# Performance work log

Hardware: AMD Instinct MI355X
Metric: run time of the kernel (lower is better)

Reference implementation:

```python
import jax, jax.numpy as jnp
import numpy as np

N_NODES = 50000
N_EDGES = 800000
IN_FEATS = 256
N_HEADS = 4
OUT_FEATS = 32
NEG_SLOPE = 0.2


def setup_inputs() -> dict:
    key = jax.random.key(0)
    k_feat, k_src, k_dst, k_fc, k_al, k_ar, k_res = jax.random.split(key, 7)
    feat = jax.random.normal(k_feat, (N_NODES, IN_FEATS), dtype=jnp.float32)
    src = jax.random.randint(k_src, (N_EDGES,), 0, N_NODES)
    dst = jax.random.randint(k_dst, (N_EDGES,), 0, N_NODES)
    # xavier-normal-ish scales
    s_fc = (2.0 / (IN_FEATS + N_HEADS * OUT_FEATS)) ** 0.5
    W_fc = jax.random.normal(k_fc, (N_HEADS * OUT_FEATS, IN_FEATS), dtype=jnp.float32) * s_fc
    s_a = (2.0 / (1 + N_HEADS * OUT_FEATS)) ** 0.5
    attn_l = jax.random.normal(k_al, (N_HEADS, OUT_FEATS), dtype=jnp.float32) * s_a
    attn_r = jax.random.normal(k_ar, (N_HEADS, OUT_FEATS), dtype=jnp.float32) * s_a
    W_res = jax.random.normal(k_res, (N_HEADS * OUT_FEATS, IN_FEATS), dtype=jnp.float32) * s_fc
    return {"feat": feat, "src": src, "dst": dst, "W_fc": W_fc,
            "attn_l": attn_l, "attn_r": attn_r, "W_res": W_res}


def reference(feat, src, dst, W_fc, attn_l, attn_r, W_res):
    N = feat.shape[0]
    H, D = attn_l.shape
    ones_e = jnp.ones(src.shape[0], dtype=feat.dtype)

    # projection: [N, H, D]
    h = (feat @ W_fc.T).reshape(N, H, D)
    feat_dst = h  # dst features are pre-norm (torch code aliases before * norm)

    # symmetric norm on source side: out_degree^-0.5
    out_deg = jax.ops.segment_sum(ones_e, src, num_segments=N)
    feat_src = h * (jnp.clip(out_deg, 1.0) ** -0.5)[:, None, None]

    # per-node attention halves -> per-edge score, leaky relu
    el = jnp.einsum('nhd,hd->nh', feat_src, attn_l)  # [N, H]
    er = jnp.einsum('nhd,hd->nh', feat_dst, attn_r)  # [N, H]
    e = jax.nn.leaky_relu(el[src] + er[dst], NEG_SLOPE)  # [E, H]

    # edge_softmax over incoming edges of each dst node
    emax = jax.ops.segment_max(e, dst, num_segments=N)
    emax = jnp.where(jnp.isfinite(emax), emax, 0.0)  # guard empty segments
    ex = jnp.exp(e - emax[dst])
    denom = jax.ops.segment_sum(ex, dst, num_segments=N)
    a = ex / denom[dst]  # [E, H]

    # weighted scatter-sum of messages: u_mul_e + sum
    msg = feat_src[src] * a[:, :, None]  # [E, H, D]
    rst = jax.ops.segment_sum(msg, dst, num_segments=N)  # [N, H, D]

    # symmetric norm on destination side: in_degree^0.5
    in_deg = jax.ops.segment_sum(ones_e, dst, num_segments=N)
    rst = rst * jnp.sqrt(jnp.clip(in_deg, 1.0))[:, None, None]

    # residual projection
    rst = rst + (feat @ W_res.T).reshape(N, H, D)
    return rst
```

## Files before the change

### kernel.cpp

```cpp
#include <hip/hip_runtime.h>
#include <hip/hip_bf16.h>
#include <math.h>

#define HD 128
#define IN_F 256
#define NEG_SLOPE 0.2f
#define NMAX 50000
#define GGRID 256
#define CSRC 32

typedef __attribute__((ext_vector_type(8))) short short8;
typedef __attribute__((ext_vector_type(4))) float f32x4;

__device__ __forceinline__ unsigned short f2bf(float x) {
    __hip_bfloat16 b = __float2bfloat16(x);
    return *(unsigned short*)&b;
}
__device__ __forceinline__ float bf2f(unsigned short u) {
    unsigned int v = ((unsigned int)u) << 16;
    float f;
    __builtin_memcpy(&f, &v, 4);
    return f;
}
__device__ __forceinline__ short8 pack8(float4 f0, float4 f1) {
    short8 v;
    v[0] = (short)f2bf(f0.x); v[1] = (short)f2bf(f0.y);
    v[2] = (short)f2bf(f0.z); v[3] = (short)f2bf(f0.w);
    v[4] = (short)f2bf(f1.x); v[5] = (short)f2bf(f1.y);
    v[6] = (short)f2bf(f1.z); v[7] = (short)f2bf(f1.w);
    return v;
}

__global__ __launch_bounds__(1024) void hist_cvt_kernel(
    const int* __restrict__ src, const int* __restrict__ dst,
    unsigned short* __restrict__ pc_src, unsigned short* __restrict__ pc_dst,
    const float4* __restrict__ wfc4, const float4* __restrict__ wres4,
    const float* __restrict__ wfc, const float* __restrict__ attn_l,
    const float* __restrict__ attn_r, ushort4* __restrict__ w16,
    unsigned short* __restrict__ ew16, int n4each,
    int N, int E, int C, int chunk, int chunk_s) {
    __shared__ unsigned int h[NMAX / 2];
    int tid = threadIdx.x;
    int b = blockIdx.x;

    if (b >= C + CSRC) {
        int rb = b - C - CSRC;
        if (rb == 0) {
            int hh = tid >> 8, k = tid & 255;
            float sl = 0.f, sr = 0.f;
#pragma unroll 8
            for (int d = 0; d < 32; d++) {
                float w = wfc[(size_t)(hh * 32 + d) * IN_F + k];
                sl += attn_l[hh * 32 + d] * w;
                sr += attn_r[hh * 32 + d] * w;
            }
            ew16[hh * IN_F + k] = f2bf(sl);
            ew16[(4 + hh) * IN_F + k] = f2bf(sr);
            ew16[(8 + hh) * IN_F + k] = 0;
            ew16[(12 + hh) * IN_F + k] = 0;
        } else {
            int idx = (rb - 1) * 1024 + tid;
            if (idx < 2 * n4each) {
                float4 f = (idx < n4each) ? wfc4[idx] : wres4[idx - n4each];
                ushort4 u;
                u.x = f2bf(f.x); u.y = f2bf(f.y); u.z = f2bf(f.z); u.w = f2bf(f.w);
                w16[idx] = u;
            }
        }
        return;
    }

    int nh = N >> 1;
    uint4* h4 = (uint4*)h;
    for (int i = tid; i < (nh >> 2); i += 1024) h4[i] = make_uint4(0, 0, 0, 0);
    for (int i = (nh & ~3) + tid; i < nh; i += 1024) h[i] = 0;
    __syncthreads();

    bool isSrc = (b >= C);
    const int* arr = isSrc ? src : dst;
    int c = isSrc ? (b - C) : b;
    int ch = isSrc ? chunk_s : chunk;
    int e0 = c * ch, e1 = min(E, (c + 1) * ch);
    for (int e = e0 + tid; e < e1; e += 1024) {
        int v = arr[e];
        atomicAdd(&h[v >> 1], 1u << ((v & 1) << 4));
    }
    __syncthreads();

    unsigned short* pc = (isSrc ? pc_src : pc_dst) + (size_t)c * N;
    uint4* pc4 = (uint4*)pc;
    for (int i = tid; i < (nh >> 2); i += 1024) pc4[i] = h4[i];
    for (int i = (nh & ~3) + tid; i < nh; i += 1024) ((unsigned int*)pc)[i] = h[i];
}

__global__ __launch_bounds__(256) void sum_scan1_kernel(
    const unsigned short* __restrict__ pc_src, unsigned short* __restrict__ pc_dst,
    int* __restrict__ out_cnt, int* __restrict__ deg, int* __restrict__ bsum,
    int N, int C) {
    __shared__ int wsum[4];
    int n = blockIdx.x * 256 + threadIdx.x;
    int sd = 0;
    if (n < N) {
        int ss = 0;
#pragma unroll 4
        for (int c = 0; c < CSRC; c++) ss += pc_src[(size_t)c * N + n];
        for (int c = 0; c < C; c++) {
            unsigned short v = pc_dst[(size_t)c * N + n];
            pc_dst[(size_t)c * N + n] = (unsigned short)sd;
            sd += v;
        }
        out_cnt[n] = ss;
        deg[n] = sd;
    }
    int v = (n < N) ? sd : 0;
#pragma unroll
    for (int d = 1; d < 64; d <<= 1) v += __shfl_xor(v, d);
    if ((threadIdx.x & 63) == 0) wsum[threadIdx.x >> 6] = v;
    __syncthreads();
    if (threadIdx.x == 0) bsum[blockIdx.x] = wsum[0] + wsum[1] + wsum[2] + wsum[3];
}

__global__ __launch_bounds__(256) void scan3_kernel(const int* __restrict__ deg,
                                                    const int* __restrict__ bsum,
                                                    int* __restrict__ row_start,
                                                    int N, int nb, int E) {
    __shared__ int wsum[4];
    __shared__ int sbo[256];
    int tid = threadIdx.x, lane = tid & 63, wid = tid >> 6;
    {
        int v = (tid < nb) ? bsum[tid] : 0;
        int incl = v;
#pragma unroll
        for (int d = 1; d < 64; d <<= 1) {
            int t = __shfl_up(incl, d);
            if (lane >= d) incl += t;
        }
        if (lane == 63) wsum[wid] = incl;
        __syncthreads();
        int woff = 0;
        for (int w = 0; w < wid; w++) woff += wsum[w];
        sbo[tid] = woff + incl - v;
        __syncthreads();
    }
    int boff = sbo[blockIdx.x];
    if (blockIdx.x == 0 && tid == 0) row_start[N] = E;
    __syncthreads();

    int i = blockIdx.x * 256 + tid;
    int v = (i < N) ? deg[i] : 0;
    int incl = v;
#pragma unroll
    for (int d = 1; d < 64; d <<= 1) {
        int t = __shfl_up(incl, d);
        if (lane >= d) incl += t;
    }
    if (lane == 63) wsum[wid] = incl;
    __syncthreads();
    int woff = 0;
    for (int w = 0; w < wid; w++) woff += wsum[w];
    int excl = boff + woff + incl - v;
    if (i < N) row_start[i] = excl;
}

__global__ __launch_bounds__(1024, 1) void place_gemm_kernel(
    const int* __restrict__ src, const int* __restrict__ dst,
    const unsigned short* __restrict__ chunkpre, const int* __restrict__ row_start,
    int* __restrict__ esrc,
    const float* __restrict__ feat, const __hip_bfloat16* __restrict__ w16,
    const __hip_bfloat16* __restrict__ ew16, const int* __restrict__ out_cnt,
    unsigned short* __restrict__ h16, unsigned short* __restrict__ resid16,
    float* __restrict__ el, float* __restrict__ er,
    int N, int E, int C, int chunk, int ntiles) {
    __shared__ __align__(16) char smem[147456];
    int tid = threadIdx.x;

    if (blockIdx.x < C) {
        unsigned int* cur = (unsigned int*)smem;
        int nh = N >> 1;
        const unsigned short* cp = chunkpre + (size_t)blockIdx.x * N;
        const uint4* cp4 = (const uint4*)cp;
        uint4* cur4 = (uint4*)cur;
        for (int i = tid; i < (nh >> 2); i += 1024) cur4[i] = cp4[i];
        for (int i = (nh & ~3) + tid; i < nh; i += 1024)
            cur[i] = ((const unsigned int*)cp)[i];
        __syncthreads();

        int e1 = min(E, (int)(blockIdx.x + 1) * chunk);
        for (int e = blockIdx.x * chunk + tid; e < e1; e += 1024) {
            int d = dst[e], s = src[e];
            int sh = (d & 1) << 4;
            unsigned int old = atomicAdd(&cur[d >> 1], 1u << sh);
            int rank = (old >> sh) & 0xffff;
            esrc[row_start[d] + rank] = s;
        }
        return;
    }

    unsigned short* sB = (unsigned short*)smem;
    unsigned short* sA = (unsigned short*)(smem + 131072);
    int bid = blockIdx.x - C;
    int lane = tid & 63, w = tid >> 6;
    int l15 = lane & 15, lg = lane >> 4;
    int c0 = w * 16;
    bool w0 = (w == 0);
    bool isH = (w < 8);
    int colloc = c0 & 127;

#pragma unroll
    for (int it = 0; it < 8; ++it) {
        int idx = it * 1024 + tid;
        int c = idx >> 5, g = idx & 31;
        short8 v = *(const short8*)(w16 + (size_t)c * IN_F + g * 8);
        *(short8*)&sB[c * 256 + ((g ^ (c & 7)) * 8)] = v;
    }
    short8 ereg[8];
    if (w0) {
        const __hip_bfloat16* ep = ew16 + (size_t)l15 * IN_F + lg * 8;
#pragma unroll
        for (int kk = 0; kk < 8; kk++) ereg[kk] = *(const short8*)(ep + kk * 32);
    }

    int srow = tid >> 5, sgc = tid & 31;
    float4 fA0, fA1;
    int t = bid;
    {
        int gm = t * 32 + srow;
        gm = (gm < N) ? gm : (N - 1);
        const float4* fp = (const float4*)(feat + (size_t)gm * IN_F + sgc * 8);
        fA0 = fp[0];
        fA1 = fp[1];
    }

    for (; t < ntiles; t += GGRID) {
        __syncthreads();
        *(short8*)&sA[srow * 256 + ((sgc ^ (srow & 7)) * 8)] = pack8(fA0, fA1);
        __syncthreads();

        int tn = t + GGRID;
        if (tn < ntiles) {
            int gm = tn * 32 + srow;
            gm = (gm < N) ? gm : (N - 1);
            const float4* fp = (const float4*)(feat + (size_t)gm * IN_F + sgc * 8);
            fA0 = fp[0];
            fA1 = fp[1];
        }

        f32x4 acc[2], accE[2];
#pragma unroll
        for (int i = 0; i < 2; i++) {
            acc[i] = (f32x4){0.f, 0.f, 0.f, 0.f};
            accE[i] = (f32x4){0.f, 0.f, 0.f, 0.f};
        }
#pragma unroll
        for (int kk = 0; kk < 8; kk++) {
            short8 a[2], b;
#pragma unroll
            for (int mi = 0; mi < 2; mi++) {
                int row = mi * 16 + l15;
                int gs = (kk * 4 + lg) ^ (row & 7);
                a[mi] = *(const short8*)&sA[row * 256 + gs * 8];
            }
            {
                int c = c0 + l15;
                int gsb = (kk * 4 + lg) ^ (c & 7);
                b = *(const short8*)&sB[c * 256 + gsb * 8];
            }
#pragma unroll
            for (int mi = 0; mi < 2; mi++)
                acc[mi] = __builtin_amdgcn_mfma_f32_16x16x32_bf16(a[mi], b, acc[mi],
                                                                  0, 0, 0);
            if (w0) {
#pragma unroll
                for (int mi = 0; mi < 2; mi++)
                    accE[mi] = __builtin_amdgcn_mfma_f32_16x16x32_bf16(
                        a[mi], ereg[kk], accE[mi], 0, 0, 0);
            }
        }

        int bm = t * 32;
#pragma unroll
        for (int mi = 0; mi < 2; mi++) {
#pragma unroll
            for (int reg = 0; reg < 4; reg++) {
                int r = bm + mi * 16 + lg * 4 + reg;
                bool valid = (r < N);
                int rr = valid ? r : 0;
                if (isH) {
                    float nrm = rsqrtf(fmaxf((float)out_cnt[rr], 1.0f));
                    if (valid) {
                        h16[(size_t)r * HD + colloc + l15] = f2bf(acc[mi][reg] * nrm);
                        if (w0) {
                            float ev = accE[mi][reg];
                            if (l15 < 4) el[r * 4 + l15] = ev * nrm;
                            else if (l15 < 8) er[r * 4 + (l15 - 4)] = ev;
                        }
                    }
                } else if (valid) {
                    resid16[(size_t)r * HD + colloc + l15] = f2bf(acc[mi][reg]);
                }
            }
        }
    }
}

__global__ __launch_bounds__(256) void agg_kernel(const unsigned short* __restrict__ h16,
                                                  const float* __restrict__ el,
                                                  const float* __restrict__ er,
                                                  const int* __restrict__ row_start,
                                                  const int* __restrict__ esrc,
                                                  const unsigned short* __restrict__ resid16,
                                                  float* __restrict__ out, int N) {
    int wid = threadIdx.x >> 6, lane = threadIdx.x & 63;
    int n = blockIdx.x * 4 + wid;
    if (n >= N) return;
    int es = lane >> 4;
    int l15 = lane & 15;
    int h = l15 >> 2;
    int d0 = l15 * 8;
    int beg = row_start[n], end = row_start[n + 1];
    float erh = er[n * 4 + h];
    float den = 0.f;
    float acc[8];
#pragma unroll
    for (int j = 0; j < 8; j++) acc[j] = 0.f;

    if (beg < end) {
        bool ok0, ok1;
        float ev0, ev1; short8 hv0, hv1;
        {
            int i0 = beg + es, i1 = beg + 4 + es;
            ok0 = i0 < end; ok1 = i1 < end;
            int s0 = esrc[ok0 ? i0 : beg];
            int s1 = esrc[ok1 ? i1 : beg];
            ev0 = el[s0 * 4 + h]; ev1 = el[s1 * 4 + h];
            hv0 = *(const short8*)(h16 + (size_t)s0 * HD + d0);
            hv1 = *(const short8*)(h16 + (size_t)s1 * HD + d0);
        }
        for (int base = beg + 8; base < end; base += 8) {
            int i0 = base + es, i1 = base + 4 + es;
            bool p0 = i0 < end, p1 = i1 < end;
            int t0 = esrc[p0 ? i0 : beg];
            int t1 = esrc[p1 ? i1 : beg];
            float fv0 = el[t0 * 4 + h];
            float fv1 = el[t1 * 4 + h];
            short8 g0 = *(const short8*)(h16 + (size_t)t0 * HD + d0);
            short8 g1 = *(const short8*)(h16 + (size_t)t1 * HD + d0);
            float e0 = ev0 + erh; e0 = (e0 > 0.f) ? e0 : NEG_SLOPE * e0;
            float e1 = ev1 + erh; e1 = (e1 > 0.f) ? e1 : NEG_SLOPE * e1;
            float ex0 = ok0 ? __expf(e0) : 0.f;
            float ex1 = ok1 ? __expf(e1) : 0.f;
            den += ex0 + ex1;
#pragma unroll
            for (int j = 0; j < 8; j++)
                acc[j] += ex0 * bf2f((unsigned short)hv0[j]) +
                          ex1 * bf2f((unsigned short)hv1[j]);
            ok0 = p0; ok1 = p1; ev0 = fv0; ev1 = fv1; hv0 = g0; hv1 = g1;
        }
        float e0 = ev0 + erh; e0 = (e0 > 0.f) ? e0 : NEG_SLOPE * e0;
        float e1 = ev1 + erh; e1 = (e1 > 0.f) ? e1 : NEG_SLOPE * e1;
        float ex0 = ok0 ? __expf(e0) : 0.f;
        float ex1 = ok1 ? __expf(e1) : 0.f;
        den += ex0 + ex1;
#pragma unroll
        for (int j = 0; j < 8; j++)
            acc[j] += ex0 * bf2f((unsigned short)hv0[j]) +
                      ex1 * bf2f((unsigned short)hv1[j]);
    }

#pragma unroll
    for (int m = 16; m < 64; m <<= 1) {
        den += __shfl_xor(den, m);
#pragma unroll
        for (int j = 0; j < 8; j++) acc[j] += __shfl_xor(acc[j], m);
    }

    if (es == 0) {
        const unsigned short* rp = resid16 + (size_t)n * HD + d0;
        short8 rv = *(const short8*)rp;
        int indeg = end - beg;
        float sc = (indeg > 0) ? sqrtf((float)indeg) / den : 0.f;
        float o[8];
#pragma unroll
        for (int j = 0; j < 8; j++)
            o[j] = sc * acc[j] + bf2f((unsigned short)rv[j]);
        float* op = out + (size_t)n * HD + d0;
        *(float4*)op = make_float4(o[0], o[1], o[2], o[3]);
        *(float4*)(op + 4) = make_float4(o[4], o[5], o[6], o[7]);
    }
}

extern "C" void kernel_launch(void* const* d_in, const int* in_sizes, int n_in,
                              void* d_out, int out_size, void* d_ws, size_t ws_size,
                              hipStream_t stream) {
    const float* feat   = (const float*)d_in[0];
    const int*   src    = (const int*)d_in[1];
    const int*   dst    = (const int*)d_in[2];
    const float* W_fc   = (const float*)d_in[3];
    const float* attn_l = (const float*)d_in[4];
    const float* attn_r = (const float*)d_in[5];
    const float* W_res  = (const float*)d_in[6];
    float* out = (float*)d_out;

    int N = in_sizes[0] / IN_F;
    int E = in_sizes[1];
    int nb = (N + 255) / 256;

    size_t off = 0;
    auto alloc = [&](size_t bytes) {
        size_t o = off;
        off = (off + bytes + 255) & ~(size_t)255;
        return o;
    };
    char* ws = (char*)d_ws;
    unsigned short* h16     = (unsigned short*)(ws + alloc((size_t)N * HD * 2));
    unsigned short* resid16 = (unsigned short*)(ws + alloc((size_t)N * HD * 2));
    __hip_bfloat16* w16     = (__hip_bfloat16*)(ws + alloc((size_t)2 * HD * IN_F * 2));
    unsigned short* ew16    = (unsigned short*)(ws + alloc((size_t)16 * IN_F * 2));
    float* el               = (float*)(ws + alloc((size_t)N * 4 * 4));
    float* er               = (float*)(ws + alloc((size_t)N * 4 * 4));
    int* out_cnt            = (int*)(ws + alloc((size_t)N * 4));
    int* deg                = (int*)(ws + alloc((size_t)N * 4));
    int* row_start          = (int*)(ws + alloc((size_t)(N + 1) * 4));
    int* bsum               = (int*)(ws + alloc((size_t)nb * 4));
    int* esrc               = (int*)(ws + alloc((size_t)E * 4));
    unsigned short* pc_src  = (unsigned short*)(ws + alloc((size_t)CSRC * N * 2));

    size_t per_chunk = (size_t)2 * N;
    size_t avail = (ws_size > off + 4096) ? (ws_size - off - 4096) : 0;
    int C = (int)(avail / per_chunk);
    if (C > 128) C = 128;
    if (C < 32) C = 32;
    unsigned short* pc_dst = (unsigned short*)(ws + alloc((size_t)C * N * 2));
    int chunk = (E + C - 1) / C;
    int chunk_s = (E + CSRC - 1) / CSRC;

    int n4each = HD * IN_F / 4;
    int cvtb = (2 * n4each + 1023) / 1024;

    hist_cvt_kernel<<<C + CSRC + 1 + cvtb, 1024, 0, stream>>>(
        src, dst, pc_src, pc_dst,
        (const float4*)W_fc, (const float4*)W_res, W_fc, attn_l, attn_r,
        (ushort4*)w16, ew16, n4each, N, E, C, chunk, chunk_s);

    sum_scan1_kernel<<<nb, 256, 0, stream>>>(pc_src, pc_dst, out_cnt, deg, bsum, N, C);
    scan3_kernel<<<nb, 256, 0, stream>>>(deg, bsum, row_start, N, nb, E);

    int ntiles = (N + 31) / 32;
    place_gemm_kernel<<<C + GGRID, 1024, 0, stream>>>(
        src, dst, pc_dst, row_start, esrc,
        feat, (const __hip_bfloat16*)w16, (const __hip_bfloat16*)ew16, out_cnt,
        h16, resid16, el, er, N, E, C, chunk, ntiles);

    int nb4 = (N + 3) / 4;
    agg_kernel<<<nb4, 256, 0, stream>>>(h16, el, er, row_start, esrc, resid16, out, N);
}
```

Before: 133.2 us.

## Merge edge placement and GEMM into one persistent grid with atomic tile scheduling

The separate placement blocks are removed. The first C blocks of a 256-block persistent grid now do their edge-placement chunk and then join the GEMM work. GEMM tiles are handed out through a global atomic counter, reset in the scan kernel, rather than by a static stride. The aim is to balance load, since blocks that finish placement early or late pick up proportionally fewer or more tiles, and to save a wave of 1024-thread blocks. The cost is one atomic per tile plus an extra barrier, and C must not exceed 256 (C is capped at 128).

New measurement: 127.4 us. 4.3% less time.

```diff
diff --git a/kernel.cpp b/kernel.cpp
--- a/kernel.cpp
+++ b/kernel.cpp
@@ -123,6 +123,7 @@
 __global__ __launch_bounds__(256) void scan3_kernel(const int* __restrict__ deg,
                                                     const int* __restrict__ bsum,
                                                     int* __restrict__ row_start,
+                                                    int* __restrict__ tilectr,
                                                     int N, int nb, int E) {
     __shared__ int wsum[4];
     __shared__ int sbo[256];
@@ -143,7 +144,10 @@
         __syncthreads();
     }
     int boff = sbo[blockIdx.x];
-    if (blockIdx.x == 0 && tid == 0) row_start[N] = E;
+    if (blockIdx.x == 0 && tid == 0) {
+        row_start[N] = E;
+        *tilectr = 0;
+    }
     __syncthreads();
 
     int i = blockIdx.x * 256 + tid;
@@ -169,12 +173,12 @@
     const float* __restrict__ feat, const __hip_bfloat16* __restrict__ w16,
     const __hip_bfloat16* __restrict__ ew16, const int* __restrict__ out_cnt,
     unsigned short* __restrict__ h16, unsigned short* __restrict__ resid16,
-    float* __restrict__ el, float* __restrict__ er,
+    float* __restrict__ el, float* __restrict__ er, int* __restrict__ tilectr,
     int N, int E, int C, int chunk, int ntiles) {
-    __shared__ __align__(16) char smem[147456];
+    __shared__ __align__(16) char smem[147520];
     int tid = threadIdx.x;
 
-    if (blockIdx.x < C) {
+    if ((int)blockIdx.x < C) {
         unsigned int* cur = (unsigned int*)smem;
         int nh = N >> 1;
         const unsigned short* cp = chunkpre + (size_t)blockIdx.x * N;
@@ -193,12 +197,12 @@
             int rank = (old >> sh) & 0xffff;
             esrc[row_start[d] + rank] = s;
         }
-        return;
+        __syncthreads();
     }
 
     unsigned short* sB = (unsigned short*)smem;
     unsigned short* sA = (unsigned short*)(smem + 131072);
-    int bid = blockIdx.x - C;
+    int* sT = (int*)(smem + 147456);
     int lane = tid & 63, w = tid >> 6;
     int l15 = lane & 15, lg = lane >> 4;
     int c0 = w * 16;
@@ -221,9 +225,12 @@
     }
 
     int srow = tid >> 5, sgc = tid & 31;
+
+    if (tid == 0) *sT = atomicAdd(tilectr, 1);
+    __syncthreads();
+    int t = *sT;
     float4 fA0, fA1;
-    int t = bid;
-    {
+    if (t < ntiles) {
         int gm = t * 32 + srow;
         gm = (gm < N) ? gm : (N - 1);
         const float4* fp = (const float4*)(feat + (size_t)gm * IN_F + sgc * 8);
@@ -231,12 +238,13 @@
         fA1 = fp[1];
     }
 
-    for (; t < ntiles; t += GGRID) {
+    while (t < ntiles) {
         __syncthreads();
         *(short8*)&sA[srow * 256 + ((sgc ^ (srow & 7)) * 8)] = pack8(fA0, fA1);
-        __syncthreads();
-
-        int tn = t + GGRID;
+        if (tid == 0) *sT = atomicAdd(tilectr, 1);
+        __syncthreads();
+
+        int tn = *sT;
         if (tn < ntiles) {
             int gm = tn * 32 + srow;
             gm = (gm < N) ? gm : (N - 1);
@@ -300,6 +308,7 @@
                 }
             }
         }
+        t = tn;
     }
 }
 
@@ -422,6 +431,7 @@
     int* deg                = (int*)(ws + alloc((size_t)N * 4));
     int* row_start          = (int*)(ws + alloc((size_t)(N + 1) * 4));
     int* bsum               = (int*)(ws + alloc((size_t)nb * 4));
+    int* tilectr            = (int*)(ws + alloc(256));
     int* esrc               = (int*)(ws + alloc((size_t)E * 4));
     unsigned short* pc_src  = (unsigned short*)(ws + alloc((size_t)CSRC * N * 2));
 
@@ -443,13 +453,13 @@
         (ushort4*)w16, ew16, n4each, N, E, C, chunk, chunk_s);
 
     sum_scan1_kernel<<<nb, 256, 0, stream>>>(pc_src, pc_dst, out_cnt, deg, bsum, N, C);
-    scan3_kernel<<<nb, 256, 0, stream>>>(deg, bsum, row_start, N, nb, E);
+    scan3_kernel<<<nb, 256, 0, stream>>>(deg, bsum, row_start, tilectr, N, nb, E);
 
     int ntiles = (N + 31) / 32;
-    place_gemm_kernel<<<C + GGRID, 1024, 0, stream>>>(
+    place_gemm_kernel<<<GGRID, 1024, 0, stream>>>(
         src, dst, pc_dst, row_start, esrc,
         feat, (const __hip_bfloat16*)w16, (const __hip_bfloat16*)ew16, out_cnt,
-        h16, resid16, el, er, N, E, C, chunk, ntiles);
+        h16, resid16, el, er, tilectr, N, E, C, chunk, ntiles);
 
     int nb4 = (N + 3) / 4;
     agg_kernel<<<nb4, 256, 0, stream>>>(h16, el, er, row_start, esrc, resid16, out, N);
```
